# Performance work log

Measured on AMD Instinct MI355X. Metric: run time of the kernel, lower is better.

The kernel has to match this reference:

```python
import jax, jax.numpy as jnp
from jax import lax
import numpy as np

LAMBDA_DAG = 0.5
B, C = 64, 5000
PARENT_PROB = 0.0008  # ~4 parents per GO term


def setup_inputs() -> dict:
    key = jax.random.key(0)
    k1, k2, k3 = jax.random.split(key, 3)
    logits = jax.random.normal(k1, (B, C), dtype=jnp.float32)
    # sparse multilabel targets (binary floats, like GO annotations)
    labels = (jax.random.uniform(k2, (B, C)) < 0.02).astype(jnp.float32)
    # sparse binary DAG adjacency: dag[i, j] = 1 if j is a parent of i
    dag = (jax.random.uniform(k3, (C, C)) < PARENT_PROB).astype(jnp.float32)
    dag = dag * (1.0 - jnp.eye(C, dtype=jnp.float32))  # no self-parents
    return {"logits": logits, "labels": labels, "dag_matrix": dag}


def reference(logits, labels, dag_matrix):
    # BCEWithLogitsLoss (mean): log(1 + exp(l)) - l * y, numerically stable
    bce = jnp.mean(jnp.logaddexp(0.0, logits) - logits * labels)

    probs = jax.nn.sigmoid(logits)                      # [B, C]
    mask = (dag_matrix > 0).astype(probs.dtype)          # [C, C]
    n_par = mask.sum(axis=1)                             # [C] parents per child

    # Accumulate sum over batch of relu(p_child - p_parent)^2 as a [C, C] matrix
    # via scan over the batch dim (keeps peak memory at one [C, C] tile).
    def body(acc, p):  # p: [C]
        d = jnp.maximum(p[:, None] - p[None, :], 0.0)
        return acc + d * d, None

    nterms = probs.shape[1]
    viol_sum, _ = lax.scan(body, jnp.zeros((nterms, nterms), probs.dtype), probs)

    # per-child-term mean over (batch, n_parents_i), only for terms with parents
    per_term = (viol_sum * mask).sum(axis=1)             # [C]
    batch = jnp.asarray(probs.shape[0], probs.dtype)
    term_mean = jnp.where(n_par > 0, per_term / (batch * jnp.maximum(n_par, 1.0)), 0.0)

    total_edges = mask.sum()
    dag_penalty = jnp.where(total_edges > 0, term_mean.sum() / jnp.maximum(total_edges, 1.0), 0.0)

    loss = bce + LAMBDA_DAG * dag_penalty
    return loss
```

## Files before the change

### kernel.cpp

```cpp
#include <hip/hip_runtime.h>
#include <math.h>

#define LAMBDA_DAG 0.5f

__global__ void k_probs_bce(const float* __restrict__ logits,
                            const float* __restrict__ labels,
                            float* __restrict__ pT,
                            float* __restrict__ bce_part,
                            int B, int C) {
    const int N = B * C;
    float acc = 0.f;
    for (int idx = blockIdx.x * blockDim.x + threadIdx.x; idx < N;
         idx += gridDim.x * blockDim.x) {
        float l = logits[idx];
        float y = labels[idx];
        acc += fmaxf(l, 0.f) + log1pf(expf(-fabsf(l))) - l * y;
        float p = 1.f / (1.f + expf(-l));
        int b = idx / C;
        int c = idx - b * C;
        pT[(size_t)c * B + b] = p;
    }
    __shared__ float sdata[256];
    sdata[threadIdx.x] = acc;
    __syncthreads();
    for (int s = blockDim.x >> 1; s > 0; s >>= 1) {
        if (threadIdx.x < s) sdata[threadIdx.x] += sdata[threadIdx.x + s];
        __syncthreads();
    }
    if (threadIdx.x == 0) bce_part[blockIdx.x] = sdata[0];
}

__global__ void __launch_bounds__(256) k_dag_rows(
        const float* __restrict__ dag,
        const float* __restrict__ pT,
        float* __restrict__ per_term,
        float* __restrict__ npar,
        int B, int C) {
    const int i = blockIdx.x;
    __shared__ float pi[128];
    for (int b = threadIdx.x; b < B; b += blockDim.x)
        pi[b] = pT[(size_t)i * B + b];
    __syncthreads();

    const float* drow = dag + (size_t)i * C;
    const int C4 = C >> 2;
    float psum = 0.f, pcnt = 0.f;

    const float4* drow4 = (const float4*)drow;
    for (int q = threadIdx.x; q < C4; q += blockDim.x) {
        float4 d4 = drow4[q];
        float dv[4] = {d4.x, d4.y, d4.z, d4.w};
#pragma unroll
        for (int k = 0; k < 4; ++k) {
            if (dv[k] > 0.f) {
                const int j = q * 4 + k;
                const float* pj = pT + (size_t)j * B;
                float s = 0.f;
                for (int b = 0; b < B; ++b) {
                    float diff = fmaxf(pi[b] - pj[b], 0.f);
                    s += diff * diff;
                }
                psum += s;
                pcnt += 1.f;
            }
        }
    }
    for (int j = C4 * 4 + threadIdx.x; j < C; j += blockDim.x) {
        if (drow[j] > 0.f) {
            const float* pj = pT + (size_t)j * B;
            float s = 0.f;
            for (int b = 0; b < B; ++b) {
                float diff = fmaxf(pi[b] - pj[b], 0.f);
                s += diff * diff;
            }
            psum += s;
            pcnt += 1.f;
        }
    }

    __shared__ float s1[256], s2[256];
    s1[threadIdx.x] = psum;
    s2[threadIdx.x] = pcnt;
    __syncthreads();
    for (int s = blockDim.x >> 1; s > 0; s >>= 1) {
        if (threadIdx.x < s) {
            s1[threadIdx.x] += s1[threadIdx.x + s];
            s2[threadIdx.x] += s2[threadIdx.x + s];
        }
        __syncthreads();
    }
    if (threadIdx.x == 0) {
        per_term[i] = s1[0];
        npar[i] = s2[0];
    }
}

__global__ void k_final(const float* __restrict__ per_term,
                        const float* __restrict__ npar,
                        const float* __restrict__ bce_part, int nb,
                        float* __restrict__ out, int B, int C) {
    float bs = 0.f, ps = 0.f, es = 0.f;
    for (int k = threadIdx.x; k < nb; k += blockDim.x) bs += bce_part[k];
    for (int i = threadIdx.x; i < C; i += blockDim.x) {
        float np = npar[i];
        es += np;
        if (np > 0.f) ps += per_term[i] / ((float)B * np);
    }
    __shared__ float s1[256], s2[256], s3[256];
    s1[threadIdx.x] = bs;
    s2[threadIdx.x] = ps;
    s3[threadIdx.x] = es;
    __syncthreads();
    for (int s = blockDim.x >> 1; s > 0; s >>= 1) {
        if (threadIdx.x < s) {
            s1[threadIdx.x] += s1[threadIdx.x + s];
            s2[threadIdx.x] += s2[threadIdx.x + s];
            s3[threadIdx.x] += s3[threadIdx.x + s];
        }
        __syncthreads();
    }
    if (threadIdx.x == 0) {
        float penalty = (s3[0] > 0.f) ? (s2[0] / s3[0]) : 0.f;
        out[0] = s1[0] / (float)(B * C) + LAMBDA_DAG * penalty;
    }
}

extern "C" void kernel_launch(void* const* d_in, const int* in_sizes, int n_in,
                              void* d_out, int out_size, void* d_ws, size_t ws_size,
                              hipStream_t stream) {
    const float* logits = (const float*)d_in[0];
    const float* labels = (const float*)d_in[1];
    const float* dag    = (const float*)d_in[2];
    float* out = (float*)d_out;

    const int C = (int)(sqrt((double)in_sizes[2]) + 0.5);
    const int B = in_sizes[0] / C;

    float* ws       = (float*)d_ws;
    float* pT       = ws;
    float* per_term = pT + (size_t)C * B;
    float* nparw    = per_term + C;
    float* bce_part = nparw + C;

    const int NB1 = 320;
    k_probs_bce<<<NB1, 256, 0, stream>>>(logits, labels, pT, bce_part, B, C);
    k_dag_rows<<<C, 256, 0, stream>>>(dag, pT, per_term, nparw, B, C);
    k_final<<<1, 256, 0, stream>>>(per_term, nparw, bce_part, NB1, out, B, C);
}
```

Before: 191.2 us.

## Flatten DAG scan across whole matrix with atomics and tile the transpose

The per-row DAG kernel, one block per child term, is replaced by a grid-stride scan over the whole C×C adjacency matrix in float4 chunks. Each nonzero edge computes its squared-violation sum with float4 loads and atomically adds the result into per-term accumulators. The probability transpose now goes through a shared-memory tile so the pT writes are coalesced, and the same kernel zeroes the accumulators. This removes the per-row reductions and the load imbalance between rows, at the cost of float atomics that make the summation order nondeterministic.

```diff
diff --git a/kernel.cpp b/kernel.cpp
--- a/kernel.cpp
+++ b/kernel.cpp
@@ -3,95 +3,138 @@
 
 #define LAMBDA_DAG 0.5f
 
-__global__ void k_probs_bce(const float* __restrict__ logits,
-                            const float* __restrict__ labels,
-                            float* __restrict__ pT,
-                            float* __restrict__ bce_part,
-                            int B, int C) {
-    const int N = B * C;
+__global__ void __launch_bounds__(256) k_probs_bce(
+        const float* __restrict__ logits,
+        const float* __restrict__ labels,
+        float* __restrict__ pT,
+        float* __restrict__ bce_part,
+        float* __restrict__ per_term,
+        float* __restrict__ npar,
+        int B, int C) {
+    for (int i = blockIdx.x * blockDim.x + threadIdx.x; i < C;
+         i += gridDim.x * blockDim.x) {
+        per_term[i] = 0.f;
+        npar[i] = 0.f;
+    }
+
+    __shared__ float tile[64][65];
+    __shared__ float sred[256];
+
+    const int c0 = blockIdx.x * 64;
     float acc = 0.f;
-    for (int idx = blockIdx.x * blockDim.x + threadIdx.x; idx < N;
-         idx += gridDim.x * blockDim.x) {
-        float l = logits[idx];
-        float y = labels[idx];
-        acc += fmaxf(l, 0.f) + log1pf(expf(-fabsf(l))) - l * y;
-        float p = 1.f / (1.f + expf(-l));
-        int b = idx / C;
-        int c = idx - b * C;
-        pT[(size_t)c * B + b] = p;
+
+    if (B <= 64 && (B & 3) == 0) {
+        const int lc = threadIdx.x & 63;
+        const int c  = c0 + lc;
+        const bool valid = (c < C);
+        for (int b = threadIdx.x >> 6; b < B; b += (blockDim.x >> 6)) {
+            float l = 0.f, y = 0.f;
+            if (valid) {
+                l = logits[(size_t)b * C + c];
+                y = labels[(size_t)b * C + c];
+                acc += fmaxf(l, 0.f) + log1pf(expf(-fabsf(l))) - l * y;
+            }
+            tile[lc][b] = 1.f / (1.f + expf(-l));
+        }
+        __syncthreads();
+        const int B4  = B >> 2;
+        const int tot = 64 * B4;
+        for (int t = threadIdx.x; t < tot; t += blockDim.x) {
+            const int row = t / B4;
+            const int q   = t - row * B4;
+            const int c2  = c0 + row;
+            if (c2 < C) {
+                float4 v;
+                v.x = tile[row][q * 4 + 0];
+                v.y = tile[row][q * 4 + 1];
+                v.z = tile[row][q * 4 + 2];
+                v.w = tile[row][q * 4 + 3];
+                *(float4*)(pT + (size_t)c2 * B + q * 4) = v;
+            }
+        }
+    } else {
+        const int N = B * C;
+        for (int idx = blockIdx.x * blockDim.x + threadIdx.x; idx < N;
+             idx += gridDim.x * blockDim.x) {
+            float l = logits[idx];
+            float y = labels[idx];
+            acc += fmaxf(l, 0.f) + log1pf(expf(-fabsf(l))) - l * y;
+            float p = 1.f / (1.f + expf(-l));
+            int b = idx / C;
+            int cc = idx - b * C;
+            pT[(size_t)cc * B + b] = p;
+        }
     }
-    __shared__ float sdata[256];
-    sdata[threadIdx.x] = acc;
+
+    sred[threadIdx.x] = acc;
     __syncthreads();
     for (int s = blockDim.x >> 1; s > 0; s >>= 1) {
-        if (threadIdx.x < s) sdata[threadIdx.x] += sdata[threadIdx.x + s];
+        if (threadIdx.x < s) sred[threadIdx.x] += sred[threadIdx.x + s];
         __syncthreads();
     }
-    if (threadIdx.x == 0) bce_part[blockIdx.x] = sdata[0];
+    if (threadIdx.x == 0) bce_part[blockIdx.x] = sred[0];
 }
 
-__global__ void __launch_bounds__(256) k_dag_rows(
+__global__ void __launch_bounds__(256) k_dag_scan(
         const float* __restrict__ dag,
         const float* __restrict__ pT,
         float* __restrict__ per_term,
         float* __restrict__ npar,
         int B, int C) {
-    const int i = blockIdx.x;
-    __shared__ float pi[128];
-    for (int b = threadIdx.x; b < B; b += blockDim.x)
-        pi[b] = pT[(size_t)i * B + b];
-    __syncthreads();
+    const size_t N  = (size_t)C * (size_t)C;
+    const size_t N4 = N >> 2;
+    const float4* dag4 = (const float4*)dag;
+    const size_t stride = (size_t)gridDim.x * blockDim.x;
+    const int B4 = B >> 2;
 
-    const float* drow = dag + (size_t)i * C;
-    const int C4 = C >> 2;
-    float psum = 0.f, pcnt = 0.f;
-
-    const float4* drow4 = (const float4*)drow;
-    for (int q = threadIdx.x; q < C4; q += blockDim.x) {
-        float4 d4 = drow4[q];
-        float dv[4] = {d4.x, d4.y, d4.z, d4.w};
+    for (size_t q = (size_t)blockIdx.x * blockDim.x + threadIdx.x; q < N4;
+         q += stride) {
+        float4 d = dag4[q];
+        if (d.x > 0.f || d.y > 0.f || d.z > 0.f || d.w > 0.f) {
+            const size_t base = q << 2;
+            float dv[4] = {d.x, d.y, d.z, d.w};
 #pragma unroll
-        for (int k = 0; k < 4; ++k) {
-            if (dv[k] > 0.f) {
-                const int j = q * 4 + k;
-                const float* pj = pT + (size_t)j * B;
-                float s = 0.f;
-                for (int b = 0; b < B; ++b) {
-                    float diff = fmaxf(pi[b] - pj[b], 0.f);
-                    s += diff * diff;
+            for (int k = 0; k < 4; ++k) {
+                if (dv[k] > 0.f) {
+                    const size_t e = base + (size_t)k;
+                    const int i = (int)(e / (size_t)C);
+                    const int j = (int)(e - (size_t)i * (size_t)C);
+                    const float4* pi4 = (const float4*)(pT + (size_t)i * B);
+                    const float4* pj4 = (const float4*)(pT + (size_t)j * B);
+                    float s = 0.f;
+                    for (int t = 0; t < B4; ++t) {
+                        float4 a = pi4[t], b = pj4[t];
+                        float d0 = fmaxf(a.x - b.x, 0.f);
+                        float d1 = fmaxf(a.y - b.y, 0.f);
+                        float d2 = fmaxf(a.z - b.z, 0.f);
+                        float d3 = fmaxf(a.w - b.w, 0.f);
+                        s += d0 * d0 + d1 * d1 + d2 * d2 + d3 * d3;
+                    }
+                    for (int b = B4 << 2; b < B; ++b) {
+                        float diff = fmaxf(pT[(size_t)i * B + b] -
+                                           pT[(size_t)j * B + b], 0.f);
+                        s += diff * diff;
+                    }
+                    atomicAdd(&per_term[i], s);
+                    atomicAdd(&npar[i], 1.f);
                 }
-                psum += s;
-                pcnt += 1.f;
             }
         }
     }
-    for (int j = C4 * 4 + threadIdx.x; j < C; j += blockDim.x) {
-        if (drow[j] > 0.f) {
-            const float* pj = pT + (size_t)j * B;
+    for (size_t e = (N4 << 2) + (size_t)blockIdx.x * blockDim.x + threadIdx.x;
+         e < N; e += stride) {
+        if (dag[e] > 0.f) {
+            const int i = (int)(e / (size_t)C);
+            const int j = (int)(e - (size_t)i * (size_t)C);
             float s = 0.f;
             for (int b = 0; b < B; ++b) {
-                float diff = fmaxf(pi[b] - pj[b], 0.f);
+                float diff = fmaxf(pT[(size_t)i * B + b] -
+                                   pT[(size_t)j * B + b], 0.f);
                 s += diff * diff;
             }
-            psum += s;
-            pcnt += 1.f;
+            atomicAdd(&per_term[i], s);
+            atomicAdd(&npar[i], 1.f);
         }
-    }
-
-    __shared__ float s1[256], s2[256];
-    s1[threadIdx.x] = psum;
-    s2[threadIdx.x] = pcnt;
-    __syncthreads();
-    for (int s = blockDim.x >> 1; s > 0; s >>= 1) {
-        if (threadIdx.x < s) {
-            s1[threadIdx.x] += s1[threadIdx.x + s];
-            s2[threadIdx.x] += s2[threadIdx.x + s];
-        }
-        __syncthreads();
-    }
-    if (threadIdx.x == 0) {
-        per_term[i] = s1[0];
-        npar[i] = s2[0];
     }
 }
 
@@ -142,8 +185,15 @@
     float* nparw    = per_term + C;
     float* bce_part = nparw + C;
 
-    const int NB1 = 320;
-    k_probs_bce<<<NB1, 256, 0, stream>>>(logits, labels, pT, bce_part, B, C);
-    k_dag_rows<<<C, 256, 0, stream>>>(dag, pT, per_term, nparw, B, C);
-    k_final<<<1, 256, 0, stream>>>(per_term, nparw, bce_part, NB1, out, B, C);
+    const int gridA = (C + 63) / 64;
+
+    k_probs_bce<<<gridA, 256, 0, stream>>>(logits, labels, pT, bce_part,
+                                           per_term, nparw, B, C);
+
+    const size_t N4 = ((size_t)C * (size_t)C) >> 2;
+    size_t needB = (N4 + 255) / 256;
+    const int gridB = (int)(needB < 2048 ? needB : 2048);
+    k_dag_scan<<<gridB, 256, 0, stream>>>(dag, pT, per_term, nparw, B, C);
+
+    k_final<<<1, 256, 0, stream>>>(per_term, nparw, bce_part, gridA, out, B, C);
 }
```

Result: slower. 210.7 us (+10.2%).
